# Kernel tuning notes

Measured on AMD Instinct MI355X. Metric: run time of the kernel, lower is better.

The kernel has to match this reference:

```python
import jax, jax.numpy as jnp
import numpy as np

V_MIN = -10.0
V_MAX = 10.0
NUM_ATOMS = 251
B = 131072
N_OBS = 128
N_ACT = 32
HID = 512


def _ln(x, g, b, eps=1e-5):
    m = jnp.mean(x, axis=-1, keepdims=True)
    v = jnp.var(x, axis=-1, keepdims=True)
    return (x - m) * jax.lax.rsqrt(v + eps) * g + b


def setup_inputs() -> dict:
    key = jax.random.key(0)
    ks = jax.random.split(key, 16)

    def lin(k, fi, fo):
        kw, kb = jax.random.split(k)
        lim = 1.0 / np.sqrt(fi)
        W = jax.random.uniform(kw, (fi, fo), jnp.float32, -lim, lim)
        b = jax.random.uniform(kb, (fo,), jnp.float32, -lim, lim)
        return W, b

    W1, b1 = lin(ks[0], N_OBS + N_ACT, HID)
    W2, b2 = lin(ks[1], HID, HID // 2)
    W3, b3 = lin(ks[2], HID // 2, HID // 4)
    W4, b4 = lin(ks[3], HID // 4, NUM_ATOMS)

    return {
        "obs": jax.random.normal(ks[4], (B, N_OBS), jnp.float32),
        "actions": jax.random.normal(ks[5], (B, N_ACT), jnp.float32),
        "rewards": jax.random.normal(ks[6], (B,), jnp.float32),
        "bootstrap": (jax.random.uniform(ks[7], (B,)) > 0.05).astype(jnp.float32),
        "discount": jnp.full((B,), 0.99, jnp.float32),
        "q_support": jnp.linspace(V_MIN, V_MAX, NUM_ATOMS, dtype=jnp.float32),
        "W1": W1, "b1": b1, "g1": jnp.ones((HID,), jnp.float32), "be1": jnp.zeros((HID,), jnp.float32),
        "W2": W2, "b2": b2, "g2": jnp.ones((HID // 2,), jnp.float32), "be2": jnp.zeros((HID // 2,), jnp.float32),
        "W3": W3, "b3": b3, "g3": jnp.ones((HID // 4,), jnp.float32), "be3": jnp.zeros((HID // 4,), jnp.float32),
        "W4": W4, "b4": b4,
    }


def _net(obs, actions, W1, b1, g1, be1, W2, b2, g2, be2, W3, b3, g3, be3, W4, b4):
    x = jnp.concatenate([obs, actions], axis=1)
    x = jax.nn.silu(_ln(x @ W1 + b1, g1, be1))
    x = jax.nn.silu(_ln(x @ W2 + b2, g2, be2))
    x = jax.nn.silu(_ln(x @ W3 + b3, g3, be3))
    return x @ W4 + b4  # [B, NUM_ATOMS] logits


def reference(obs, actions, rewards, bootstrap, discount, q_support,
              W1, b1, g1, be1, W2, b2, g2, be2, W3, b3, g3, be3, W4, b4):
    # C51 categorical projection (DistributionalQNetwork.projection)
    delta_z = (V_MAX - V_MIN) / (NUM_ATOMS - 1)
    bsz = rewards.shape[0]
    target_z = rewards[:, None] + bootstrap[:, None] * discount[:, None] * q_support[None, :]
    target_z = jnp.clip(target_z, V_MIN, V_MAX)
    b = (target_z - V_MIN) / delta_z  # fractional bin positions [B, A]
    lower = jnp.floor(b).astype(jnp.int32)
    upper = jnp.ceil(b).astype(jnp.int32)
    is_integer = upper == lower
    lower_mask = (lower > 0) & is_integer
    upper_mask = (lower == 0) & is_integer
    lower = jnp.where(lower_mask, lower - 1, lower)
    upper = jnp.where(upper_mask, upper + 1, upper)

    logits = _net(obs, actions, W1, b1, g1, be1, W2, b2, g2, be2, W3, b3, g3, be3, W4, b4)
    next_dist = jax.nn.softmax(logits, axis=1)

    offset = (jnp.arange(bsz, dtype=jnp.int32) * NUM_ATOMS)[:, None]  # [B,1]
    max_index = bsz * NUM_ATOMS - 1
    li = jnp.clip((lower + offset).reshape(-1), 0, max_index)
    ui = jnp.clip((upper + offset).reshape(-1), 0, max_index)

    w_lo = (next_dist * (upper.astype(jnp.float32) - b)).reshape(-1)
    w_hi = (next_dist * (b - lower.astype(jnp.float32))).reshape(-1)

    proj = jnp.zeros((bsz * NUM_ATOMS,), next_dist.dtype)
    proj = proj.at[li].add(w_lo).at[ui].add(w_hi)
    return proj.reshape(bsz, NUM_ATOMS)
```

## Files before the change

kernel.cpp:

```cpp
#include <hip/hip_runtime.h>


#define THREADS 256
#define PREP_THREADS 256

typedef __attribute__((ext_vector_type(8))) short short8v;
typedef __attribute__((ext_vector_type(4))) float f32x4;

__device__ __forceinline__ unsigned short f2bf(float f) {
  union { float f; unsigned u; } v; v.f = f;
  unsigned u = v.u;
  u += 0x7fffu + ((u >> 16) & 1u);
  return (unsigned short)(u >> 16);
}
__device__ __forceinline__ unsigned pack2bf(float a, float b) {
  unsigned r;
  asm("v_cvt_pk_bf16_f32 %0, %1, %2" : "=v"(r) : "v"(a), "v"(b));
  return r;
}

__global__ void prep_kernel(const float* __restrict__ W1, const float* __restrict__ W2,
                            const float* __restrict__ W3, const float* __restrict__ W4,
                            unsigned short* __restrict__ ws) {
  int i = blockIdx.x * PREP_THREADS + threadIdx.x;
  if (i < 81920) {
    int n = i / 160, k = i - n * 160;
    ws[i] = f2bf(W1[k * 512 + n]);
  } else if (i < 212992) {
    int j = i - 81920; int n = j >> 9, k = j & 511;
    ws[i] = f2bf(W2[k * 256 + n]);
  } else if (i < 245760) {
    int j = i - 212992; int n = j >> 8, k = j & 255;
    ws[i] = f2bf(W3[k * 128 + n]);
  } else if (i < 278528) {
    int j = i - 245760; int n = j >> 7, k = j & 127;
    ws[i] = (n < 251) ? f2bf(W4[k * 251 + n]) : (unsigned short)0;
  }
}

#define OFF_R   0
#define OFF_ZS  16384
#define OFF_B4  17408
#define OFF_RED 18432
#define LDS_TOTAL 19008

template<int KD, int NFT>
__device__ __forceinline__ void gemm_w(const unsigned short* __restrict__ WT,
                                       const unsigned char* __restrict__ Hb,
                                       int fbase, f32x4 (&acc)[NFT]) {
  const int lane = threadIdx.x & 63;
  const int lm = lane & 15, kg = lane >> 4;
  constexpr int KS  = KD / 32;
  constexpr int G   = (NFT > 4) ? 2 : 1;
  constexpr int FPG = NFT / G;
  constexpr int NIT = KS * G;

  const int woff0 = (fbase + lm) * KD + kg * 8;
  const int r = lm;
  const int swz = (r & 7) << 4;
  const int bbase = r * (KD * 2) + kg * 16;
  const int boff0 = bbase ^ swz;
  const int boff1 = (bbase + 64) ^ swz;

  short8v abuf[2][FPG];
  short8v bbuf[2];
  bbuf[0] = *(const short8v*)(Hb + boff0);
#pragma unroll
  for (int f = 0; f < FPG; ++f)
    abuf[0][f] = *(const short8v*)(WT + woff0 + f * (16 * KD));

#pragma unroll
  for (int it = 0; it < NIT; ++it) {
    const int ks = it / G, g = it % G;
    const int cur = it & 1, nxt = cur ^ 1;
    if (it + 1 < NIT) {
      const int nit = it + 1;
      const int nks = nit / G, ng = nit % G;
      if (ng == 0) {
        const int koff = (nks >> 1) * 128;
        bbuf[nks & 1] = *(const short8v*)(Hb + ((nks & 1) ? boff1 : boff0) + koff);
      }
#pragma unroll
      for (int f = 0; f < FPG; ++f)
        abuf[nxt][f] = *(const short8v*)(WT + woff0 + (ng * FPG + f) * (16 * KD) + nks * 32);
    }
#pragma unroll
    for (int f = 0; f < FPG; ++f) {
      const int ft = g * FPG + f;
      acc[ft] = __builtin_amdgcn_mfma_f32_16x16x32_bf16(abuf[cur][f], bbuf[ks & 1], acc[ft], 0, 0, 0);
    }
  }
}

template<int ND, int NFT>
__device__ __forceinline__ void ln_silu_store(
    f32x4 (&acc)[NFT],
    const float* __restrict__ bias, const float* __restrict__ g,
    const float* __restrict__ be, unsigned char* __restrict__ Hb,
    float* __restrict__ redL, int fbase, int fq)
{
  const int lane = threadIdx.x & 63;
  const int lm = lane & 15, kg = lane >> 4;
  float s = 0.f, q = 0.f;
#pragma unroll
  for (int ft = 0; ft < NFT; ++ft) {
    const int f0 = fbase + ft * 16 + kg * 4;
    const f32x4 bb = *(const f32x4*)(bias + f0);
#pragma unroll
    for (int rg = 0; rg < 4; ++rg) {
      float x = acc[ft][rg] + bb[rg];
      acc[ft][rg] = x;
      s += x; q += x * x;
    }
  }
  s += __shfl_xor(s, 16); s += __shfl_xor(s, 32);
  q += __shfl_xor(q, 16); q += __shfl_xor(q, 32);
  if (lane < 16) {
    redL[lm * 9 + fq * 2    ] = s;
    redL[lm * 9 + fq * 2 + 1] = q;
  }
  __syncthreads();
  float S = 0.f, Q = 0.f;
#pragma unroll
  for (int w = 0; w < 4; ++w) {
    S += redL[lm * 9 + w * 2];
    Q += redL[lm * 9 + w * 2 + 1];
  }
  const float mean = S * (1.0f / ND);
  const float var  = Q * (1.0f / ND) - mean * mean;
  const float rstd = rsqrtf(var + 1e-5f);
#pragma unroll
  for (int ft = 0; ft < NFT; ++ft) {
    const int f0 = fbase + ft * 16 + kg * 4;
    const f32x4 g4 = *(const f32x4*)(g + f0);
    const f32x4 e4 = *(const f32x4*)(be + f0);
    float h[4];
#pragma unroll
    for (int rg = 0; rg < 4; ++rg) {
      float y = (acc[ft][rg] - mean) * rstd * g4[rg] + e4[rg];
      h[rg] = y * (1.0f / (1.0f + __expf(-y)));
    }
    uint2 w; w.x = pack2bf(h[0], h[1]); w.y = pack2bf(h[2], h[3]);
    int byte = lm * (ND * 2) + f0 * 2;
    byte ^= ((lm & 7) << 4);
    *(uint2*)(Hb + byte) = w;
  }
}

__global__ __launch_bounds__(THREADS, 6) void fused_kernel(
    const float* __restrict__ obs, const float* __restrict__ actions,
    const float* __restrict__ rewards, const float* __restrict__ bootstrap,
    const float* __restrict__ discount, const float* __restrict__ q_support,
    const float* __restrict__ b1, const float* __restrict__ g1, const float* __restrict__ be1,
    const float* __restrict__ b2, const float* __restrict__ g2, const float* __restrict__ be2,
    const float* __restrict__ b3, const float* __restrict__ g3, const float* __restrict__ be3,
    const float* __restrict__ b4,
    const unsigned short* __restrict__ ws,
    float* __restrict__ out)
{
  __shared__ __align__(16) unsigned char smem[LDS_TOTAL];
  const int tid  = threadIdx.x;
  const int fq   = tid >> 6;
  const int lane = tid & 63;
  const int lm   = lane & 15;
  const int kg   = lane >> 4;
  const int row0 = blockIdx.x * 16;

  const unsigned short* W1T = ws;
  const unsigned short* W2T = ws + 81920;
  const unsigned short* W3T = ws + 212992;
  const unsigned short* W4T = ws + 245760;

  float* zsL  = (float*)(smem + OFF_ZS);
  float* b4L  = (float*)(smem + OFF_B4);
  float* redL = (float*)(smem + OFF_RED);

  const int rr = row0 + lm;
  const float rw = rewards[rr];
  const float bt = bootstrap[rr];
  const float dc = discount[rr];

  zsL[tid] = (tid < 251) ? q_support[tid] : 0.f;
  b4L[tid] = (tid < 251) ? b4[tid] : 0.f;

  {
    unsigned char* Xb = smem + OFF_R;
    for (int qq = tid; qq < 640; qq += THREADS) {
      const int r  = qq / 40;
      const int c4 = (qq - r * 40) * 4;
      float4 v;
      if (c4 < 128) v = *(const float4*)(obs + (size_t)(row0 + r) * 128 + c4);
      else          v = *(const float4*)(actions + (size_t)(row0 + r) * 32 + (c4 - 128));
      uint2 w; w.x = pack2bf(v.x, v.y); w.y = pack2bf(v.z, v.w);
      int byte = r * 320 + c4 * 2;
      byte ^= ((r & 7) << 4);
      *(uint2*)(Xb + byte) = w;
    }
  }
  __syncthreads();

  f32x4 acc1[8];
#pragma unroll
  for (int i = 0; i < 8; ++i) acc1[i] = f32x4{0.f, 0.f, 0.f, 0.f};
  gemm_w<160, 8>(W1T, smem + OFF_R, fq * 128, acc1);
  ln_silu_store<512, 8>(acc1, b1, g1, be1, smem + OFF_R, redL, fq * 128, fq);
  __syncthreads();

  f32x4 acc2[4];
#pragma unroll
  for (int i = 0; i < 4; ++i) acc2[i] = f32x4{0.f, 0.f, 0.f, 0.f};
  gemm_w<512, 4>(W2T, smem + OFF_R, fq * 64, acc2);
  ln_silu_store<256, 4>(acc2, b2, g2, be2, smem + OFF_R, redL, fq * 64, fq);
  __syncthreads();

  f32x4 acc3[2];
  acc3[0] = f32x4{0.f, 0.f, 0.f, 0.f};
  acc3[1] = f32x4{0.f, 0.f, 0.f, 0.f};
  gemm_w<256, 2>(W3T, smem + OFF_R, fq * 32, acc3);
  ln_silu_store<128, 2>(acc3, b3, g3, be3, smem + OFF_R, redL, fq * 32, fq);
  __syncthreads();

  f32x4 acc4[4];
#pragma unroll
  for (int i = 0; i < 4; ++i) acc4[i] = f32x4{0.f, 0.f, 0.f, 0.f};
  gemm_w<128, 4>(W4T, smem + OFF_R, fq * 64, acc4);

  float lv[4][4];
#pragma unroll
  for (int ft = 0; ft < 4; ++ft) {
    const int f0 = fq * 64 + ft * 16 + kg * 4;
    const f32x4 bb = *(const f32x4*)(b4L + f0);
#pragma unroll
    for (int rg = 0; rg < 4; ++rg) {
      const int f = f0 + rg;
      lv[ft][rg] = (f < 251) ? (acc4[ft][rg] + bb[rg]) : -1e30f;
    }
  }

  {
    float m = lv[0][0];
#pragma unroll
    for (int ft = 0; ft < 4; ++ft)
#pragma unroll
      for (int rg = 0; rg < 4; ++rg) m = fmaxf(m, lv[ft][rg]);
    m = fmaxf(m, __shfl_xor(m, 16));
    m = fmaxf(m, __shfl_xor(m, 32));
    if (lane < 16) redL[lm * 5 + fq] = m;
  }
  __syncthreads();

  float* projL = (float*)(smem + OFF_R);
  for (int i = tid; i < 16 * 251; i += THREADS) projL[i] = 0.f;

  float gm;
  {
    float m = redL[lm * 5];
#pragma unroll
    for (int w = 1; w < 4; ++w) m = fmaxf(m, redL[lm * 5 + w]);
    gm = m;
  }
  __syncthreads();
  {
    float E = 0.f;
#pragma unroll
    for (int ft = 0; ft < 4; ++ft)
#pragma unroll
      for (int rg = 0; rg < 4; ++rg) {
        float e = __expf(lv[ft][rg] - gm);
        lv[ft][rg] = e;
        E += e;
      }
    E += __shfl_xor(E, 16); E += __shfl_xor(E, 32);
    if (lane < 16) redL[lm * 5 + fq] = E;
  }
  __syncthreads();
  float inv;
  {
    float E = 0.f;
#pragma unroll
    for (int w = 0; w < 4; ++w) E += redL[lm * 5 + w];
    inv = 1.0f / E;
  }

  constexpr float DZF = 20.0f / 250.0f;
  const int base = lm * 251;
  const float bd = __fmul_rn(bt, dc);
#pragma unroll
  for (int ft = 0; ft < 4; ++ft) {
    const int f0 = fq * 64 + ft * 16 + kg * 4;
    const f32x4 z4 = *(const f32x4*)(zsL + f0);
#pragma unroll
    for (int rg = 0; rg < 4; ++rg) {
      const int f = f0 + rg;
      if (f < 251) {
        const float p = lv[ft][rg] * inv;
        float t = __fadd_rn(rw, __fmul_rn(bd, z4[rg]));
        t = fminf(fmaxf(t, -10.0f), 10.0f);
        const float bfr = __fdiv_rn(__fsub_rn(t, -10.0f), DZF);
        const float fl = floorf(bfr), fu = ceilf(bfr);
        int l = (int)fl, u = (int)fu;
        if (fl == fu) { if (l > 0) --l; else ++u; }
        atomicAdd(projL + base + l, p * ((float)u - bfr));
        atomicAdd(projL + base + u, p * (bfr - (float)l));
      }
    }
  }
  __syncthreads();

  const float4* ps = (const float4*)projL;
  float4* po = (float4*)(out + (size_t)row0 * 251);
  for (int i = tid; i < 1004; i += THREADS) po[i] = ps[i];
}

extern "C" void kernel_launch(void* const* d_in, const int* in_sizes, int n_in,
                              void* d_out, int out_size, void* d_ws, size_t ws_size,
                              hipStream_t stream) {
  const float* obs  = (const float*)d_in[0];
  const float* act  = (const float*)d_in[1];
  const float* rew  = (const float*)d_in[2];
  const float* boot = (const float*)d_in[3];
  const float* disc = (const float*)d_in[4];
  const float* zs   = (const float*)d_in[5];
  const float* W1   = (const float*)d_in[6];
  const float* b1   = (const float*)d_in[7];
  const float* g1   = (const float*)d_in[8];
  const float* be1  = (const float*)d_in[9];
  const float* W2   = (const float*)d_in[10];
  const float* b2   = (const float*)d_in[11];
  const float* g2   = (const float*)d_in[12];
  const float* be2  = (const float*)d_in[13];
  const float* W3   = (const float*)d_in[14];
  const float* b3   = (const float*)d_in[15];
  const float* g3   = (const float*)d_in[16];
  const float* be3  = (const float*)d_in[17];
  const float* W4   = (const float*)d_in[18];
  const float* b4   = (const float*)d_in[19];
  unsigned short* wsp = (unsigned short*)d_ws;

  const int Bn = in_sizes[2];
  prep_kernel<<<(278528 + PREP_THREADS - 1) / PREP_THREADS, PREP_THREADS, 0, stream>>>(
      W1, W2, W3, W4, wsp);
  fused_kernel<<<Bn / 16, THREADS, 0, stream>>>(obs, act, rew, boot, disc, zs,
      b1, g1, be1, b2, g2, be2, b3, g3, be3, b4, wsp, (float*)d_out);
}
```

Measured before the change: 554.3 us.

## Give each wave a full 16-row tile through all layers, dropping block syncs

Work is now split by rows instead of by output features. Each wave owns 16 rows and computes every output feature of every layer, so the LayerNorm and softmax reductions happen inside one wave with shuffles, and the block-wide barriers become per-wave LDS waitcnt fences. Blocks shrink to 2 waves and the GEMM uses an 8-deep rolling prefetch of weight fragments, and the bin-position divide becomes a multiply by the reciprocal. The cost is very large accumulator arrays per wave (up to 32 f32x4 tiles), which raises register pressure and cuts occupancy, and each wave now streams the whole weight set from cache by itself.

```diff
diff --git a/kernel.cpp b/kernel.cpp
--- a/kernel.cpp
+++ b/kernel.cpp
@@ -1,7 +1,7 @@
 #include <hip/hip_runtime.h>
 
 
-#define THREADS 256
+#define THREADS 128
 #define PREP_THREADS 256
 
 typedef __attribute__((ext_vector_type(8))) short short8v;
@@ -17,6 +17,11 @@
   unsigned r;
   asm("v_cvt_pk_bf16_f32 %0, %1, %2" : "=v"(r) : "v"(a), "v"(b));
   return r;
+}
+
+__device__ __forceinline__ void lds_fence() {
+  asm volatile("s_waitcnt lgkmcnt(0)" ::: "memory");
+  __builtin_amdgcn_sched_barrier(0);
 }
 
 __global__ void prep_kernel(const float* __restrict__ W1, const float* __restrict__ W2,
@@ -38,73 +43,63 @@
   }
 }
 
-#define OFF_R   0
-#define OFF_ZS  16384
-#define OFF_B4  17408
-#define OFF_RED 18432
-#define LDS_TOTAL 19008
-
-template<int KD, int NFT>
-__device__ __forceinline__ void gemm_w(const unsigned short* __restrict__ WT,
-                                       const unsigned char* __restrict__ Hb,
-                                       int fbase, f32x4 (&acc)[NFT]) {
+template<int KD, int NT>
+__device__ __forceinline__ void gemm_wave(const unsigned short* __restrict__ WT,
+                                          const unsigned char* __restrict__ Hb,
+                                          f32x4 (&acc)[NT]) {
+  constexpr int KS = KD / 32, NIT = KS * NT;
   const int lane = threadIdx.x & 63;
   const int lm = lane & 15, kg = lane >> 4;
-  constexpr int KS  = KD / 32;
-  constexpr int G   = (NFT > 4) ? 2 : 1;
-  constexpr int FPG = NFT / G;
-  constexpr int NIT = KS * G;
-
-  const int woff0 = (fbase + lm) * KD + kg * 8;
-  const int r = lm;
-  const int swz = (r & 7) << 4;
-  const int bbase = r * (KD * 2) + kg * 16;
-  const int boff0 = bbase ^ swz;
-  const int boff1 = (bbase + 64) ^ swz;
-
-  short8v abuf[2][FPG];
-  short8v bbuf[2];
-  bbuf[0] = *(const short8v*)(Hb + boff0);
-#pragma unroll
-  for (int f = 0; f < FPG; ++f)
-    abuf[0][f] = *(const short8v*)(WT + woff0 + f * (16 * KD));
-
-#pragma unroll
-  for (int it = 0; it < NIT; ++it) {
-    const int ks = it / G, g = it % G;
-    const int cur = it & 1, nxt = cur ^ 1;
-    if (it + 1 < NIT) {
-      const int nit = it + 1;
-      const int nks = nit / G, ng = nit % G;
-      if (ng == 0) {
-        const int koff = (nks >> 1) * 128;
-        bbuf[nks & 1] = *(const short8v*)(Hb + ((nks & 1) ? boff1 : boff0) + koff);
+  const int swz = (lm & 7) << 4;
+  const int bbase = lm * (KD * 2) + kg * 16;
+  const int boffE = bbase ^ swz;
+  const int boffO = (bbase + 64) ^ swz;
+  const int woff = lm * KD + kg * 8;
+
+  short8v abuf[8];
+  short8v bcur, bnxt;
+
+  bcur = *(const short8v*)(Hb + boffE);
+  if constexpr (KS > 1) bnxt = *(const short8v*)(Hb + boffO);
+#pragma unroll
+  for (int f = 0; f < 8; ++f)
+    abuf[f] = *(const short8v*)(WT + woff + f * (16 * KD));
+
+#pragma unroll
+  for (int ks = 0; ks < KS; ++ks) {
+#pragma unroll
+    for (int ft = 0; ft < NT; ++ft) {
+      acc[ft] = __builtin_amdgcn_mfma_f32_16x16x32_bf16(abuf[ft & 7], bcur,
+                                                        acc[ft], 0, 0, 0);
+      const int nit = ks * NT + ft + 8;
+      if (nit < NIT) {
+        const int nks = nit / NT, nf = nit % NT;
+        abuf[ft & 7] =
+            *(const short8v*)(WT + woff + nf * (16 * KD) + nks * 32);
       }
-#pragma unroll
-      for (int f = 0; f < FPG; ++f)
-        abuf[nxt][f] = *(const short8v*)(WT + woff0 + (ng * FPG + f) * (16 * KD) + nks * 32);
-    }
-#pragma unroll
-    for (int f = 0; f < FPG; ++f) {
-      const int ft = g * FPG + f;
-      acc[ft] = __builtin_amdgcn_mfma_f32_16x16x32_bf16(abuf[cur][f], bbuf[ks & 1], acc[ft], 0, 0, 0);
-    }
-  }
-}
-
-template<int ND, int NFT>
+    }
+    if (ks + 1 < KS) {
+      bcur = bnxt;
+      if (ks + 2 < KS) {
+        const int a = ((ks + 2) & 1) ? boffO : boffE;
+        bnxt = *(const short8v*)(Hb + a + ((ks + 2) >> 1) * 128);
+      }
+    }
+  }
+}
+
+template<int ND, int NT>
 __device__ __forceinline__ void ln_silu_store(
-    f32x4 (&acc)[NFT],
+    f32x4 (&acc)[NT],
     const float* __restrict__ bias, const float* __restrict__ g,
-    const float* __restrict__ be, unsigned char* __restrict__ Hb,
-    float* __restrict__ redL, int fbase, int fq)
+    const float* __restrict__ be, unsigned char* __restrict__ Hb)
 {
   const int lane = threadIdx.x & 63;
   const int lm = lane & 15, kg = lane >> 4;
   float s = 0.f, q = 0.f;
 #pragma unroll
-  for (int ft = 0; ft < NFT; ++ft) {
-    const int f0 = fbase + ft * 16 + kg * 4;
+  for (int ft = 0; ft < NT; ++ft) {
+    const int f0 = ft * 16 + kg * 4;
     const f32x4 bb = *(const f32x4*)(bias + f0);
 #pragma unroll
     for (int rg = 0; rg < 4; ++rg) {
@@ -115,23 +110,12 @@
   }
   s += __shfl_xor(s, 16); s += __shfl_xor(s, 32);
   q += __shfl_xor(q, 16); q += __shfl_xor(q, 32);
-  if (lane < 16) {
-    redL[lm * 9 + fq * 2    ] = s;
-    redL[lm * 9 + fq * 2 + 1] = q;
-  }
-  __syncthreads();
-  float S = 0.f, Q = 0.f;
-#pragma unroll
-  for (int w = 0; w < 4; ++w) {
-    S += redL[lm * 9 + w * 2];
-    Q += redL[lm * 9 + w * 2 + 1];
-  }
-  const float mean = S * (1.0f / ND);
-  const float var  = Q * (1.0f / ND) - mean * mean;
+  const float mean = s * (1.0f / ND);
+  const float var  = q * (1.0f / ND) - mean * mean;
   const float rstd = rsqrtf(var + 1e-5f);
 #pragma unroll
-  for (int ft = 0; ft < NFT; ++ft) {
-    const int f0 = fbase + ft * 16 + kg * 4;
+  for (int ft = 0; ft < NT; ++ft) {
+    const int f0 = ft * 16 + kg * 4;
     const f32x4 g4 = *(const f32x4*)(g + f0);
     const f32x4 e4 = *(const f32x4*)(be + f0);
     float h[4];
@@ -141,13 +125,12 @@
       h[rg] = y * (1.0f / (1.0f + __expf(-y)));
     }
     uint2 w; w.x = pack2bf(h[0], h[1]); w.y = pack2bf(h[2], h[3]);
-    int byte = lm * (ND * 2) + f0 * 2;
-    byte ^= ((lm & 7) << 4);
+    const int byte = (lm * (ND * 2) + f0 * 2) ^ ((lm & 7) << 4);
     *(uint2*)(Hb + byte) = w;
   }
 }
 
-__global__ __launch_bounds__(THREADS, 6) void fused_kernel(
+__global__ __launch_bounds__(THREADS, 2) void fused_kernel(
     const float* __restrict__ obs, const float* __restrict__ actions,
     const float* __restrict__ rewards, const float* __restrict__ bootstrap,
     const float* __restrict__ discount, const float* __restrict__ q_support,
@@ -158,145 +141,126 @@
     const unsigned short* __restrict__ ws,
     float* __restrict__ out)
 {
-  __shared__ __align__(16) unsigned char smem[LDS_TOTAL];
+  __shared__ __align__(16) unsigned char smem[32768];
   const int tid  = threadIdx.x;
-  const int fq   = tid >> 6;
+  const int wid  = tid >> 6;
   const int lane = tid & 63;
   const int lm   = lane & 15;
   const int kg   = lane >> 4;
-  const int row0 = blockIdx.x * 16;
+  const int row0 = (blockIdx.x * 2 + wid) * 16;
+  unsigned char* R = smem + wid * 16384;
 
   const unsigned short* W1T = ws;
   const unsigned short* W2T = ws + 81920;
   const unsigned short* W3T = ws + 212992;
   const unsigned short* W4T = ws + 245760;
 
-  float* zsL  = (float*)(smem + OFF_ZS);
-  float* b4L  = (float*)(smem + OFF_B4);
-  float* redL = (float*)(smem + OFF_RED);
-
-  const int rr = row0 + lm;
-  const float rw = rewards[rr];
-  const float bt = bootstrap[rr];
-  const float dc = discount[rr];
-
-  zsL[tid] = (tid < 251) ? q_support[tid] : 0.f;
-  b4L[tid] = (tid < 251) ? b4[tid] : 0.f;
-
-  {
-    unsigned char* Xb = smem + OFF_R;
-    for (int qq = tid; qq < 640; qq += THREADS) {
-      const int r  = qq / 40;
-      const int c4 = (qq - r * 40) * 4;
-      float4 v;
-      if (c4 < 128) v = *(const float4*)(obs + (size_t)(row0 + r) * 128 + c4);
-      else          v = *(const float4*)(actions + (size_t)(row0 + r) * 32 + (c4 - 128));
-      uint2 w; w.x = pack2bf(v.x, v.y); w.y = pack2bf(v.z, v.w);
-      int byte = r * 320 + c4 * 2;
-      byte ^= ((r & 7) << 4);
-      *(uint2*)(Xb + byte) = w;
-    }
-  }
-  __syncthreads();
-
-  f32x4 acc1[8];
-#pragma unroll
-  for (int i = 0; i < 8; ++i) acc1[i] = f32x4{0.f, 0.f, 0.f, 0.f};
-  gemm_w<160, 8>(W1T, smem + OFF_R, fq * 128, acc1);
-  ln_silu_store<512, 8>(acc1, b1, g1, be1, smem + OFF_R, redL, fq * 128, fq);
-  __syncthreads();
-
-  f32x4 acc2[4];
-#pragma unroll
-  for (int i = 0; i < 4; ++i) acc2[i] = f32x4{0.f, 0.f, 0.f, 0.f};
-  gemm_w<512, 4>(W2T, smem + OFF_R, fq * 64, acc2);
-  ln_silu_store<256, 4>(acc2, b2, g2, be2, smem + OFF_R, redL, fq * 64, fq);
-  __syncthreads();
-
-  f32x4 acc3[2];
-  acc3[0] = f32x4{0.f, 0.f, 0.f, 0.f};
-  acc3[1] = f32x4{0.f, 0.f, 0.f, 0.f};
-  gemm_w<256, 2>(W3T, smem + OFF_R, fq * 32, acc3);
-  ln_silu_store<128, 2>(acc3, b3, g3, be3, smem + OFF_R, redL, fq * 32, fq);
-  __syncthreads();
-
-  f32x4 acc4[4];
-#pragma unroll
-  for (int i = 0; i < 4; ++i) acc4[i] = f32x4{0.f, 0.f, 0.f, 0.f};
-  gemm_w<128, 4>(W4T, smem + OFF_R, fq * 64, acc4);
-
-  float lv[4][4];
-#pragma unroll
-  for (int ft = 0; ft < 4; ++ft) {
-    const int f0 = fq * 64 + ft * 16 + kg * 4;
-    const f32x4 bb = *(const f32x4*)(b4L + f0);
+#pragma unroll
+  for (int i = 0; i < 10; ++i) {
+    const int qq = i * 64 + lane;
+    const int r  = qq / 40;
+    const int c4 = (qq - r * 40) * 4;
+    float4 v;
+    if (c4 < 128) v = *(const float4*)(obs + (size_t)(row0 + r) * 128 + c4);
+    else          v = *(const float4*)(actions + (size_t)(row0 + r) * 32 + (c4 - 128));
+    uint2 w; w.x = pack2bf(v.x, v.y); w.y = pack2bf(v.z, v.w);
+    const int byte = (r * 320 + c4 * 2) ^ ((r & 7) << 4);
+    *(uint2*)(R + byte) = w;
+  }
+  lds_fence();
+
+  f32x4 acc1[32];
+#pragma unroll
+  for (int i = 0; i < 32; ++i) acc1[i] = f32x4{0.f, 0.f, 0.f, 0.f};
+  gemm_wave<160, 32>(W1T, R, acc1);
+  lds_fence();
+  ln_silu_store<512, 32>(acc1, b1, g1, be1, R);
+  lds_fence();
+
+  f32x4 acc2[16];
+#pragma unroll
+  for (int i = 0; i < 16; ++i) acc2[i] = f32x4{0.f, 0.f, 0.f, 0.f};
+  gemm_wave<512, 16>(W2T, R, acc2);
+  lds_fence();
+  ln_silu_store<256, 16>(acc2, b2, g2, be2, R);
+  lds_fence();
+
+  f32x4 acc3[8];
+#pragma unroll
+  for (int i = 0; i < 8; ++i) acc3[i] = f32x4{0.f, 0.f, 0.f, 0.f};
+  gemm_wave<256, 8>(W3T, R, acc3);
+  lds_fence();
+  ln_silu_store<128, 8>(acc3, b3, g3, be3, R);
+  lds_fence();
+
+  f32x4 acc4[16];
+#pragma unroll
+  for (int i = 0; i < 16; ++i) acc4[i] = f32x4{0.f, 0.f, 0.f, 0.f};
+  gemm_wave<128, 16>(W4T, R, acc4);
+
+#pragma unroll
+  for (int ft = 0; ft < 16; ++ft) {
+    const int f0 = ft * 16 + kg * 4;
+    if (ft < 15) {
+      const f32x4 bv = *(const f32x4*)(b4 + f0);
+#pragma unroll
+      for (int rg = 0; rg < 4; ++rg) acc4[ft][rg] += bv[rg];
+    } else {
+#pragma unroll
+      for (int rg = 0; rg < 4; ++rg) {
+        const int f = f0 + rg;
+        acc4[ft][rg] = (f < 251) ? (acc4[ft][rg] + b4[f]) : -1e30f;
+      }
+    }
+  }
+
+  float m = -1e30f;
+#pragma unroll
+  for (int ft = 0; ft < 16; ++ft)
+#pragma unroll
+    for (int rg = 0; rg < 4; ++rg) m = fmaxf(m, acc4[ft][rg]);
+  m = fmaxf(m, __shfl_xor(m, 16));
+  m = fmaxf(m, __shfl_xor(m, 32));
+  float E = 0.f;
+#pragma unroll
+  for (int ft = 0; ft < 16; ++ft)
 #pragma unroll
     for (int rg = 0; rg < 4; ++rg) {
-      const int f = f0 + rg;
-      lv[ft][rg] = (f < 251) ? (acc4[ft][rg] + bb[rg]) : -1e30f;
-    }
-  }
-
-  {
-    float m = lv[0][0];
-#pragma unroll
-    for (int ft = 0; ft < 4; ++ft)
-#pragma unroll
-      for (int rg = 0; rg < 4; ++rg) m = fmaxf(m, lv[ft][rg]);
-    m = fmaxf(m, __shfl_xor(m, 16));
-    m = fmaxf(m, __shfl_xor(m, 32));
-    if (lane < 16) redL[lm * 5 + fq] = m;
-  }
-  __syncthreads();
-
-  float* projL = (float*)(smem + OFF_R);
-  for (int i = tid; i < 16 * 251; i += THREADS) projL[i] = 0.f;
-
-  float gm;
-  {
-    float m = redL[lm * 5];
-#pragma unroll
-    for (int w = 1; w < 4; ++w) m = fmaxf(m, redL[lm * 5 + w]);
-    gm = m;
-  }
-  __syncthreads();
-  {
-    float E = 0.f;
-#pragma unroll
-    for (int ft = 0; ft < 4; ++ft)
-#pragma unroll
-      for (int rg = 0; rg < 4; ++rg) {
-        float e = __expf(lv[ft][rg] - gm);
-        lv[ft][rg] = e;
-        E += e;
-      }
-    E += __shfl_xor(E, 16); E += __shfl_xor(E, 32);
-    if (lane < 16) redL[lm * 5 + fq] = E;
-  }
-  __syncthreads();
-  float inv;
-  {
-    float E = 0.f;
-#pragma unroll
-    for (int w = 0; w < 4; ++w) E += redL[lm * 5 + w];
-    inv = 1.0f / E;
-  }
+      const float e = __expf(acc4[ft][rg] - m);
+      acc4[ft][rg] = e;
+      E += e;
+    }
+  E += __shfl_xor(E, 16); E += __shfl_xor(E, 32);
+  const float inv = 1.0f / E;
+
+  lds_fence();
+  float4* Rz = (float4*)R;
+  for (int i = lane; i < 1004; i += 64) Rz[i] = float4{0.f, 0.f, 0.f, 0.f};
+  lds_fence();
+
+  const float rw = rewards[row0 + lm];
+  const float bt = bootstrap[row0 + lm];
+  const float dc = discount[row0 + lm];
+  const float bd = __fmul_rn(bt, dc);
 
   constexpr float DZF = 20.0f / 250.0f;
+  constexpr float INVDZ = 1.0f / DZF;
+  float* projL = (float*)R;
   const int base = lm * 251;
-  const float bd = __fmul_rn(bt, dc);
-#pragma unroll
-  for (int ft = 0; ft < 4; ++ft) {
-    const int f0 = fq * 64 + ft * 16 + kg * 4;
-    const f32x4 z4 = *(const f32x4*)(zsL + f0);
+#pragma unroll
+  for (int ft = 0; ft < 16; ++ft) {
+    const int f0 = ft * 16 + kg * 4;
+    f32x4 z4 = f32x4{0.f, 0.f, 0.f, 0.f};
+    if (ft < 15) z4 = *(const f32x4*)(q_support + f0);
 #pragma unroll
     for (int rg = 0; rg < 4; ++rg) {
       const int f = f0 + rg;
       if (f < 251) {
-        const float p = lv[ft][rg] * inv;
-        float t = __fadd_rn(rw, __fmul_rn(bd, z4[rg]));
+        const float z = (ft < 15) ? z4[rg] : q_support[f];
+        const float p = acc4[ft][rg] * inv;
+        float t = __fadd_rn(rw, __fmul_rn(bd, z));
         t = fminf(fmaxf(t, -10.0f), 10.0f);
-        const float bfr = __fdiv_rn(__fsub_rn(t, -10.0f), DZF);
+        const float bfr = __fmul_rn(__fsub_rn(t, -10.0f), INVDZ);
         const float fl = floorf(bfr), fu = ceilf(bfr);
         int l = (int)fl, u = (int)fu;
         if (fl == fu) { if (l > 0) --l; else ++u; }
@@ -305,11 +269,11 @@
       }
     }
   }
-  __syncthreads();
-
-  const float4* ps = (const float4*)projL;
+  lds_fence();
+
+  const float4* ps = (const float4*)R;
   float4* po = (float4*)(out + (size_t)row0 * 251);
-  for (int i = tid; i < 1004; i += THREADS) po[i] = ps[i];
+  for (int i = lane; i < 1004; i += 64) po[i] = ps[i];
 }
 
 extern "C" void kernel_launch(void* const* d_in, const int* in_sizes, int n_in,
@@ -340,6 +304,6 @@
   const int Bn = in_sizes[2];
   prep_kernel<<<(278528 + PREP_THREADS - 1) / PREP_THREADS, PREP_THREADS, 0, stream>>>(
       W1, W2, W3, W4, wsp);
-  fused_kernel<<<Bn / 16, THREADS, 0, stream>>>(obs, act, rew, boot, disc, zs,
+  fused_kernel<<<Bn / 32, THREADS, 0, stream>>>(obs, act, rew, boot, disc, zs,
       b1, g1, be1, b2, g2, be2, b3, g3, be3, b4, wsp, (float*)d_out);
 }
```

After: 782.5 us. +41.2%, slower.
